# Kernel optimization log

Hardware: AMD Instinct MI355X
Metric: run time of the kernel (lower is better)

Reference implementation:

```python
import jax, jax.numpy as jnp
import numpy as np

B, S, D = 1, 2048, 6144
H, KV, HD = 48, 8, 128  # query heads, kv heads, head dim
THETA = 10000.0


def _rope_tables(seq_len, head_dim, theta):
    pos = jnp.arange(seq_len, dtype=jnp.float32)
    inv_freq = 1.0 / (theta ** (jnp.arange(0, head_dim, 2, dtype=jnp.float32) / head_dim))
    freqs = pos[:, None] * inv_freq[None, :]                 # [S, HD/2]
    emb = jnp.concatenate([freqs, freqs], axis=-1)           # [S, HD]
    return jnp.cos(emb), jnp.sin(emb)


def setup_inputs() -> dict:
    key = jax.random.key(0)
    k1, k2, k3 = jax.random.split(key, 3)
    hidden_states = jax.random.normal(k1, (B, S, D), dtype=jnp.float32) * 0.02
    w_qkv = jax.random.normal(k2, (D, (H + 2 * KV) * HD), dtype=jnp.float32) * 0.02
    w_out = jax.random.normal(k3, (H * HD, D), dtype=jnp.float32) * 0.02
    cos, sin = _rope_tables(S, HD, THETA)
    return {"hidden_states": hidden_states, "cos": cos, "sin": sin,
            "w_qkv": w_qkv, "w_out": w_out}


def _rotate_half(x):
    x1, x2 = jnp.split(x, 2, axis=-1)
    return jnp.concatenate([-x2, x1], axis=-1)


def reference(hidden_states, cos, sin, w_qkv, w_out):
    b, s, d = hidden_states.shape
    # fused QKV projection
    qkv = jnp.einsum('bsd,de->bse', hidden_states, w_qkv)
    q = qkv[..., : H * HD].reshape(b, s, H, HD)
    k = qkv[..., H * HD: (H + KV) * HD].reshape(b, s, KV, HD)
    v = qkv[..., (H + KV) * HD:].reshape(b, s, KV, HD)
    # rotary embedding (rotate-half form)
    c = cos[None, :, None, :]
    sn = sin[None, :, None, :]
    q = q * c + _rotate_half(q) * sn
    k = k * c + _rotate_half(k) * sn
    # GQA: expand kv heads to query heads
    rep = H // KV
    k = jnp.repeat(k, rep, axis=2)  # [b, s, H, HD]
    v = jnp.repeat(v, rep, axis=2)
    scale = 1.0 / jnp.sqrt(jnp.float32(HD))
    scores = jnp.einsum('bqhd,bkhd->bhqk', q, k) * scale     # [b,H,S,S]
    causal = jnp.tril(jnp.ones((s, s), dtype=bool))
    scores = jnp.where(causal[None, None], scores, jnp.float32(-1e30))
    attn = jax.nn.softmax(scores, axis=-1)
    out = jnp.einsum('bhqk,bkhd->bqhd', attn, v).reshape(b, s, H * HD)
    return jnp.einsum('bsd,de->bse', out, w_out)
```

## Files before the change

kernel.cpp:

```cpp
#include <hip/hip_runtime.h>


#define S_   2048
#define D_   6144
#define H_   48
#define KV_  8
#define HD_  128
#define NQK  8192
#define REP  6

typedef __attribute__((ext_vector_type(8)))  __bf16 bf16x8;
typedef __attribute__((ext_vector_type(4)))  __bf16 bf16x4;
typedef __attribute__((ext_vector_type(2)))  __bf16 bf16x2;
typedef __attribute__((ext_vector_type(4)))  float  f32x4;
typedef __attribute__((ext_vector_type(16))) float  f32x16;
typedef __attribute__((ext_vector_type(4)))  float  float4v;

__device__ __forceinline__ void gl_lds16(const void* g, void* l) {
  __builtin_amdgcn_global_load_lds(
      (const __attribute__((address_space(1))) void*)g,
      (__attribute__((address_space(3))) void*)l, 16, 0, 0);
}

__device__ __forceinline__ unsigned pack2(float a, float b) {
  union { bf16x2 v; unsigned u; } x;
  x.v[0] = (__bf16)a; x.v[1] = (__bf16)b;
  return x.u;
}

__global__ __launch_bounds__(256) void cvt_bf16(const float* __restrict__ in,
                                                __bf16* __restrict__ out, int n4) {
  int stride = gridDim.x * 256;
  for (int i = blockIdx.x * 256 + threadIdx.x; i < n4; i += stride) {
    float4v v = ((const float4v*)in)[i];
    bf16x4 o;
    o[0] = (__bf16)v[0]; o[1] = (__bf16)v[1];
    o[2] = (__bf16)v[2]; o[3] = (__bf16)v[3];
    ((bf16x4*)out)[i] = o;
  }
}

__global__ __launch_bounds__(256) void wtrans(const float* __restrict__ src,
                                              __bf16* __restrict__ dst,
                                              int K, int N) {
  __shared__ float t[64][37];
  const int n0 = blockIdx.x * 32, k0 = blockIdx.y * 64;
  const int tid = threadIdx.x;
  const int kr = tid >> 3, nc = (tid & 7) * 4;
#pragma unroll
  for (int i = 0; i < 2; ++i) {
    float4v v = *(const float4v*)(src + (size_t)(k0 + kr + i * 32) * N + n0 + nc);
    t[kr + i * 32][nc + 0] = v[0];
    t[kr + i * 32][nc + 1] = v[1];
    t[kr + i * 32][nc + 2] = v[2];
    t[kr + i * 32][nc + 3] = v[3];
  }
  __syncthreads();
  const int nr = tid >> 3, kc = (tid & 7) * 8;
  bf16x8 o;
#pragma unroll
  for (int j = 0; j < 8; ++j) o[j] = (__bf16)t[kc + j][nr];
  *(bf16x8*)(dst + (size_t)(n0 + nr) * K + k0 + kc) = o;
}

template <typename CT, int BN>
__global__ __launch_bounds__(512, 2) void gemm_bt(const __bf16* __restrict__ A,
                                                  const __bf16* __restrict__ BT,
                                                  CT* __restrict__ C,
                                                  int M, int N, int K) {
  constexpr int NB = BN / 64;
  constexpr int NF = BN / 64;
  __shared__ __align__(16) __bf16 As[2][256 * 64];
  __shared__ __align__(16) __bf16 Bs[2][BN * 64];
  const int tid = threadIdx.x;
  const int w = tid >> 6, l = tid & 63;
  const int lr = l & 15, lg = l >> 4;
  const int wm = w >> 2, wn = w & 3;
  const int nwg = gridDim.x * gridDim.y;
  int bid = blockIdx.y * gridDim.x + blockIdx.x;
  bid = (bid & 7) * (nwg >> 3) + (bid >> 3);
  const int m0 = (bid / gridDim.x) * 256, n0 = (bid % gridDim.x) * BN;
  const int nkt = K >> 6;

  auto stage_all = [&](int T) {
    const int buf = T & 1, k0 = T << 6;
#pragma unroll
    for (int j = 0; j < 4; ++j) {
      int idx = j * 512 + tid;
      int row = idx >> 3;
      int c = (idx & 7) ^ (row & 7);
      gl_lds16(A + (size_t)(m0 + row) * K + k0 + c * 8,
               As[buf] + (size_t)(j * 512 + w * 64) * 8);
    }
#pragma unroll
    for (int j = 0; j < NB; ++j) {
      int idx = j * 512 + tid;
      int row = idx >> 3;
      int c = (idx & 7) ^ (row & 7);
      gl_lds16(BT + (size_t)(n0 + row) * K + k0 + c * 8,
               Bs[buf] + (size_t)(j * 512 + w * 64) * 8);
    }
  };
  auto rdA = [&](const __bf16* Ab, int mh, int kk, bf16x8* afr) {
#pragma unroll
    for (int m = 0; m < 4; ++m) {
      int row = wm * 128 + (mh * 4 + m) * 16 + lr;
      afr[m] = *(const bf16x8*)(Ab + (size_t)row * 64
                                + (((kk * 4 + lg) ^ (lr & 7)) * 8));
    }
  };
  auto rdB = [&](const __bf16* Bb, int kk, bf16x8* bfr) {
#pragma unroll
    for (int n = 0; n < NF; ++n) {
      int row = wn * (BN / 4) + n * 16 + lr;
      bfr[n] = *(const bf16x8*)(Bb + (size_t)row * 64
                                + (((kk * 4 + lg) ^ (lr & 7)) * 8));
    }
  };
#define SBAR  __builtin_amdgcn_s_barrier()
#define MFMA_CLUSTER(ACC_OFF)                                                   \
  __builtin_amdgcn_s_setprio(1);                                               \
  _Pragma("unroll")                                                             \
  for (int m = 0; m < 4; ++m)                                                   \
    _Pragma("unroll")                                                           \
    for (int n = 0; n < NF; ++n)                                                \
      acc[(ACC_OFF) + m][n] = __builtin_amdgcn_mfma_f32_16x16x32_bf16(          \
          afr[m], bfr[n], acc[(ACC_OFF) + m][n], 0, 0, 0);                      \
  __builtin_amdgcn_s_setprio(0)

  f32x4 acc[8][NF] = {};
  stage_all(0);
  asm volatile("s_waitcnt vmcnt(0)" ::: "memory");
  SBAR;

  for (int T = 0; T < nkt; ++T) {
    const __bf16* Ab = As[T & 1];
    const __bf16* Bb = Bs[T & 1];
    bf16x8 afr[4], bfr[NF];
    rdA(Ab, 0, 0, afr);
    rdB(Bb, 0, bfr);
    if (T + 1 < nkt) stage_all(T + 1);
    MFMA_CLUSTER(0);
    SBAR;
    rdA(Ab, 1, 0, afr);
    MFMA_CLUSTER(4);
    SBAR;
    rdA(Ab, 0, 1, afr);
    rdB(Bb, 1, bfr);
    MFMA_CLUSTER(0);
    SBAR;
    rdA(Ab, 1, 1, afr);
    MFMA_CLUSTER(4);
    asm volatile("s_waitcnt lgkmcnt(0)" ::: "memory");
    if (T + 1 < nkt) asm volatile("s_waitcnt vmcnt(0)" ::: "memory");
    SBAR;
  }
#undef SBAR
#undef MFMA_CLUSTER
#pragma unroll
  for (int m = 0; m < 8; ++m)
#pragma unroll
    for (int n = 0; n < NF; ++n)
#pragma unroll
      for (int j = 0; j < 4; ++j) {
        int row = m0 + wm * 128 + m * 16 + lg * 4 + j;
        int col = n0 + wn * (BN / 4) + n * 16 + lr;
        C[(size_t)row * N + col] = (CT)acc[m][n][j];
      }
}

template <typename CT>
__global__ __launch_bounds__(512, 2) void gemm2_bt(const __bf16* __restrict__ A,
                                                   const __bf16* __restrict__ BT,
                                                   CT* __restrict__ C,
                                                   int M, int N, int K) {
  __shared__ __align__(16) __bf16 As[2][128 * 64];
  __shared__ __align__(16) __bf16 Bs[2][192 * 64];
  const int tid = threadIdx.x;
  const int w = tid >> 6, l = tid & 63;
  const int lr = l & 15, lg = l >> 4;
  const int wm = w >> 2, wn = w & 3;
  const int nwg = gridDim.x * gridDim.y;
  int bid = blockIdx.y * gridDim.x + blockIdx.x;
  bid = (bid & 7) * (nwg >> 3) + (bid >> 3);
  const int m0 = (bid / gridDim.x) * 128, n0 = (bid % gridDim.x) * 192;
  const int nkt = K >> 6;

  auto stage_all = [&](int T) {
    const int buf = T & 1, k0 = T << 6;
#pragma unroll
    for (int j = 0; j < 2; ++j) {
      int idx = j * 512 + tid;
      int row = idx >> 3;
      int c = (idx & 7) ^ (row & 7);
      gl_lds16(A + (size_t)(m0 + row) * K + k0 + c * 8,
               As[buf] + (size_t)(j * 512 + w * 64) * 8);
    }
#pragma unroll
    for (int j = 0; j < 3; ++j) {
      int idx = j * 512 + tid;
      int row = idx >> 3;
      int c = (idx & 7) ^ (row & 7);
      gl_lds16(BT + (size_t)(n0 + row) * K + k0 + c * 8,
               Bs[buf] + (size_t)(j * 512 + w * 64) * 8);
    }
  };
  auto rdA = [&](const __bf16* Ab, int kk, bf16x8* afr) {
#pragma unroll
    for (int m = 0; m < 4; ++m) {
      int row = wm * 64 + m * 16 + lr;
      afr[m] = *(const bf16x8*)(Ab + (size_t)row * 64
                                + (((kk * 4 + lg) ^ (lr & 7)) * 8));
    }
  };
  auto rdB = [&](const __bf16* Bb, int kk, bf16x8* bfr) {
#pragma unroll
    for (int n = 0; n < 3; ++n) {
      int row = wn * 48 + n * 16 + lr;
      bfr[n] = *(const bf16x8*)(Bb + (size_t)row * 64
                                + (((kk * 4 + lg) ^ (lr & 7)) * 8));
    }
  };

  f32x4 acc[4][3] = {};
  stage_all(0);
  asm volatile("s_waitcnt vmcnt(0)" ::: "memory");
  __builtin_amdgcn_s_barrier();

  for (int T = 0; T < nkt; ++T) {
    const __bf16* Ab = As[T & 1];
    const __bf16* Bb = Bs[T & 1];
    bf16x8 afr[4], bfr[3];
    rdA(Ab, 0, afr);
    rdB(Bb, 0, bfr);
    if (T + 1 < nkt) stage_all(T + 1);
    __builtin_amdgcn_s_setprio(1);
#pragma unroll
    for (int m = 0; m < 4; ++m)
#pragma unroll
      for (int n = 0; n < 3; ++n)
        acc[m][n] = __builtin_amdgcn_mfma_f32_16x16x32_bf16(afr[m], bfr[n], acc[m][n], 0, 0, 0);
    __builtin_amdgcn_s_setprio(0);
    __builtin_amdgcn_s_barrier();
    rdA(Ab, 1, afr);
    rdB(Bb, 1, bfr);
    __builtin_amdgcn_s_setprio(1);
#pragma unroll
    for (int m = 0; m < 4; ++m)
#pragma unroll
      for (int n = 0; n < 3; ++n)
        acc[m][n] = __builtin_amdgcn_mfma_f32_16x16x32_bf16(afr[m], bfr[n], acc[m][n], 0, 0, 0);
    __builtin_amdgcn_s_setprio(0);
    asm volatile("s_waitcnt lgkmcnt(0)" ::: "memory");
    if (T + 1 < nkt) asm volatile("s_waitcnt vmcnt(0)" ::: "memory");
    __builtin_amdgcn_s_barrier();
  }
#pragma unroll
  for (int m = 0; m < 4; ++m)
#pragma unroll
    for (int n = 0; n < 3; ++n)
#pragma unroll
      for (int j = 0; j < 4; ++j) {
        int row = m0 + wm * 64 + m * 16 + lg * 4 + j;
        int col = n0 + wn * 48 + n * 16 + lr;
        C[(size_t)row * N + col] = (CT)acc[m][n][j];
      }
}

__global__ __launch_bounds__(256) void rope_qk(const __bf16* __restrict__ qkv,
                                               const float* __restrict__ cosT,
                                               const float* __restrict__ sinT,
                                               __bf16* __restrict__ Qo,
                                               __bf16* __restrict__ Ko) {
  const int s = blockIdx.x;
  const __bf16* base = qkv + (size_t)s * NQK;
  const float* ct = cosT + s * HD_;
  const float* st = sinT + s * HD_;
  const float scale = 0.1275174313f;
  for (int q4 = threadIdx.x; q4 < H_ * HD_ / 4; q4 += 256) {
    int h = q4 >> 5, d = (q4 & 31) * 4;
    bf16x4 x  = *(const bf16x4*)(base + h * HD_ + d);
    bf16x4 xr = (d < 64) ? *(const bf16x4*)(base + h * HD_ + d + 64)
                         : *(const bf16x4*)(base + h * HD_ + d - 64);
    float4v c4 = *(const float4v*)(ct + d);
    float4v s4 = *(const float4v*)(st + d);
    bf16x4 o;
#pragma unroll
    for (int j = 0; j < 4; ++j) {
      float r = (d < 64) ? -(float)xr[j] : (float)xr[j];
      o[j] = (__bf16)(((float)x[j] * c4[j] + r * s4[j]) * scale);
    }
    *(bf16x4*)(Qo + ((size_t)s * H_ + h) * HD_ + d) = o;
  }
  for (int q4 = threadIdx.x; q4 < KV_ * HD_ / 4; q4 += 256) {
    int h = q4 >> 5, d = (q4 & 31) * 4;
    const __bf16* kb = base + H_ * HD_;
    bf16x4 x  = *(const bf16x4*)(kb + h * HD_ + d);
    bf16x4 xr = (d < 64) ? *(const bf16x4*)(kb + h * HD_ + d + 64)
                         : *(const bf16x4*)(kb + h * HD_ + d - 64);
    float4v c4 = *(const float4v*)(ct + d);
    float4v s4 = *(const float4v*)(st + d);
    bf16x4 o;
#pragma unroll
    for (int j = 0; j < 4; ++j) {
      float r = (d < 64) ? -(float)xr[j] : (float)xr[j];
      o[j] = (__bf16)((float)x[j] * c4[j] + r * s4[j]);
    }
    *(bf16x4*)(Ko + ((size_t)s * KV_ + h) * HD_ + d) = o;
  }
}

__global__ __launch_bounds__(256) void v_trans(const __bf16* __restrict__ qkv,
                                               __bf16* __restrict__ Vt) {
  __shared__ __bf16 t[32][36];
  const int s0 = blockIdx.x * 32, d0 = blockIdx.y * 32, h = blockIdx.z;
  const int tx = threadIdx.x, ty = threadIdx.y;
  *(bf16x4*)&t[ty][tx * 4] =
      *(const bf16x4*)(qkv + (size_t)(s0 + ty) * NQK + (H_ + KV_) * HD_ + h * HD_ + d0 + tx * 4);
  __syncthreads();
  bf16x4 o;
#pragma unroll
  for (int j = 0; j < 4; ++j) o[j] = t[tx * 4 + j][ty];
  *(bf16x4*)(Vt + ((size_t)h * HD_ + d0 + ty) * S_ + s0 + tx * 4) = o;
}

__global__ __launch_bounds__(256, 2) void attn(const __bf16* __restrict__ Q,
                                               const __bf16* __restrict__ Kb,
                                               const __bf16* __restrict__ Vt,
                                               __bf16* __restrict__ O) {
  __shared__ __align__(16) __bf16 Ks[2][64 * 128];
  __shared__ __align__(16) __bf16 Vs[2][128 * 64];
  const int bx = blockIdx.x, h = blockIdx.y, kvh = h / REP;
  const int tid = threadIdx.x, w = tid >> 6, l = tid & 63;
  const int c = l & 31, g = l >> 5;
  const int qb = bx * 128;
  const int qrow = qb + w * 32 + c;
  const int tmax_w = (qb + w * 32 + 31) >> 6;
  const int NT = (qb >> 6) + 2;

  auto stage = [&](int t) {
    const int buf = t & 1;
    const int kbase = t << 6;
#pragma unroll
    for (int j = 0; j < 4; ++j) {
      int idx = j * 256 + tid;
      int row = idx >> 4, cc = (idx & 15) ^ (row & 15);
      gl_lds16(Kb + ((size_t)(kbase + row) * KV_ + kvh) * HD_ + cc * 8,
               Ks[buf] + (size_t)(j * 256 + w * 64) * 8);
    }
#pragma unroll
    for (int j = 0; j < 4; ++j) {
      int idx = j * 256 + tid;
      int row = idx >> 3, cc = (idx & 7) ^ (row & 7);
      gl_lds16(Vt + (size_t)(kvh * HD_ + row) * S_ + kbase + cc * 8,
               Vs[buf] + (size_t)(j * 256 + w * 64) * 8);
    }
  };

  bf16x8 qf[8];
  const __bf16* qp = Q + ((size_t)qrow * H_ + h) * HD_ + g * 8;
#pragma unroll
  for (int st = 0; st < 8; ++st) qf[st] = *(const bf16x8*)(qp + st * 16);

  f32x16 o[4] = {};
  float m = -1e30f, lsum = 0.f;

  stage(0);
  __syncthreads();
  for (int t = 0; t < NT; ++t) {
    const int buf = t & 1;
    if (t + 1 < NT) stage(t + 1);
    if (t <= tmax_w) {
      const int kbase = t << 6;
      f32x16 s0 = {}, s1 = {};
      __builtin_amdgcn_s_setprio(1);
#pragma unroll
      for (int st = 0; st < 8; ++st) {
        int ch = ((st * 2 + g) ^ (c & 15)) * 8;
        bf16x8 k0 = *(const bf16x8*)(Ks[buf] + (size_t)c * 128 + ch);
        bf16x8 k1 = *(const bf16x8*)(Ks[buf] + (size_t)(32 + c) * 128 + ch);
        s0 = __builtin_amdgcn_mfma_f32_32x32x16_bf16(k0, qf[st], s0, 0, 0, 0);
        s1 = __builtin_amdgcn_mfma_f32_32x32x16_bf16(k1, qf[st], s1, 0, 0, 0);
      }
      __builtin_amdgcn_s_setprio(0);
      if (t == tmax_w) {
#pragma unroll
        for (int r = 0; r < 16; ++r) {
          int krow = (r & 3) + 8 * (r >> 2) + 4 * g;
          if (kbase + krow > qrow)      s0[r] = -1e30f;
          if (kbase + 32 + krow > qrow) s1[r] = -1e30f;
        }
      }
      float mj = s0[0];
#pragma unroll
      for (int r = 1; r < 16; ++r) mj = fmaxf(mj, s0[r]);
#pragma unroll
      for (int r = 0; r < 16; ++r) mj = fmaxf(mj, s1[r]);
      mj = fmaxf(mj, __shfl_xor(mj, 32));
      float mnew = fmaxf(m, mj);
      float sc = __builtin_amdgcn_exp2f(m - mnew);
      float rs = 0.f;
      float p0[16], p1[16];
#pragma unroll
      for (int r = 0; r < 16; ++r) { p0[r] = __builtin_amdgcn_exp2f(s0[r] - mnew); rs += p0[r]; }
#pragma unroll
      for (int r = 0; r < 16; ++r) { p1[r] = __builtin_amdgcn_exp2f(s1[r] - mnew); rs += p1[r]; }
      rs += __shfl_xor(rs, 32);
      lsum = lsum * sc + rs;
      m = mnew;
#pragma unroll
      for (int db = 0; db < 4; ++db)
#pragma unroll
        for (int r = 0; r < 16; ++r) o[db][r] *= sc;
      unsigned bq[4][4];
#pragma unroll
      for (int n = 0; n < 2; ++n)
#pragma unroll
        for (int tq = 0; tq < 2; ++tq) {
          const float* pp = n ? p1 : p0;
          unsigned q0 = pack2(pp[8 * tq + 0], pp[8 * tq + 1]);
          unsigned q1 = pack2(pp[8 * tq + 2], pp[8 * tq + 3]);
          unsigned q2 = pack2(pp[8 * tq + 4], pp[8 * tq + 5]);
          unsigned q3 = pack2(pp[8 * tq + 6], pp[8 * tq + 7]);
          unsigned v0 = g ? q0 : q2;
          unsigned v1 = g ? q1 : q3;
          unsigned sh0 = (unsigned)__shfl_xor((int)v0, 32);
          unsigned sh1 = (unsigned)__shfl_xor((int)v1, 32);
          int s = n * 2 + tq;
          bq[s][0] = g ? sh0 : q0;
          bq[s][1] = g ? sh1 : q1;
          bq[s][2] = g ? q2 : sh0;
          bq[s][3] = g ? q3 : sh1;
        }
      __builtin_amdgcn_s_setprio(1);
#pragma unroll
      for (int s = 0; s < 4; ++s) {
        union { unsigned u[4]; bf16x8 v; } bb;
        bb.u[0] = bq[s][0]; bb.u[1] = bq[s][1]; bb.u[2] = bq[s][2]; bb.u[3] = bq[s][3];
#pragma unroll
        for (int db = 0; db < 4; ++db) {
          int ch = ((s * 2 + g) ^ (c & 7)) * 8;
          bf16x8 vfr = *(const bf16x8*)(Vs[buf] + (size_t)(db * 32 + c) * 64 + ch);
          o[db] = __builtin_amdgcn_mfma_f32_32x32x16_bf16(vfr, bb.v, o[db], 0, 0, 0);
        }
      }
      __builtin_amdgcn_s_setprio(0);
    }
    if (t + 1 < NT) __syncthreads();
  }
  float inv = 1.f / lsum;
#pragma unroll
  for (int db = 0; db < 4; ++db)
#pragma unroll
    for (int rg = 0; rg < 4; ++rg) {
      bf16x4 ov;
#pragma unroll
      for (int j = 0; j < 4; ++j) ov[j] = (__bf16)(o[db][rg * 4 + j] * inv);
      *(bf16x4*)(O + (size_t)qrow * D_ + h * HD_ + db * 32 + rg * 8 + g * 4) = ov;
    }
}

extern "C" void kernel_launch(void* const* d_in, const int* in_sizes, int n_in,
                              void* d_out, int out_size, void* d_ws, size_t ws_size,
                              hipStream_t stream) {
  const float* hidden = (const float*)d_in[0];
  const float* cosT   = (const float*)d_in[1];
  const float* sinT   = (const float*)d_in[2];
  const float* w_qkv  = (const float*)d_in[3];
  const float* w_out  = (const float*)d_in[4];
  float* out = (float*)d_out;
  char* ws = (char*)d_ws;

  __bf16* wT   = (__bf16*)ws;
  __bf16* hb   = (__bf16*)(ws + 100663296);
  __bf16* qkvb = (__bf16*)(ws + 100663296 + 25165824);
  __bf16* q_b  = (__bf16*)(ws + 100663296 + 25165824 + 33554432);
  __bf16* k_b  = q_b + (size_t)S_ * H_ * HD_;
  __bf16* vt_b = k_b + (size_t)S_ * KV_ * HD_;

  cvt_bf16<<<dim3(2048), dim3(256), 0, stream>>>(hidden, hb, (int)((size_t)S_ * D_ / 4));
  wtrans<<<dim3(NQK / 32, D_ / 64), dim3(256), 0, stream>>>(w_qkv, wT, D_, NQK);
  gemm_bt<__bf16, 256><<<dim3(NQK / 256, S_ / 256), dim3(512), 0, stream>>>(hb, wT, qkvb, S_, NQK, D_);
  rope_qk<<<dim3(S_), dim3(256), 0, stream>>>(qkvb, cosT, sinT, q_b, k_b);
  v_trans<<<dim3(S_ / 32, HD_ / 32, KV_), dim3(8, 32), 0, stream>>>(qkvb, vt_b);
  wtrans<<<dim3(D_ / 32, D_ / 64), dim3(256), 0, stream>>>(w_out, wT, D_, D_);
  attn<<<dim3(S_ / 128, H_), dim3(256), 0, stream>>>(q_b, k_b, vt_b, hb);
  gemm2_bt<float><<<dim3(D_ / 192, S_ / 128), dim3(512), 0, stream>>>(hb, wT, out, S_, D_, D_);
}
```

Measured before the change: 628.4 us.

## Restructure QKV GEMM into 8-phase half-K staged pipeline

Replaces the QKV projection GEMM with a variant that splits each 64-wide K tile into two 32-wide halves, each in its own LDS buffer. Loads for later tiles are issued in finer-grained pieces across eight MFMA phases per two K tiles, waiting with vmcnt(4) instead of draining all loads. The LDS swizzle changes to fit 32-element rows. The goal is to keep more global loads in flight and overlap them better with MFMA work, at the cost of more barriers per iteration and more complex synchronisation.

```diff
diff --git a/kernel.cpp b/kernel.cpp
--- a/kernel.cpp
+++ b/kernel.cpp
@@ -63,15 +63,13 @@
   *(bf16x8*)(dst + (size_t)(n0 + nr) * K + k0 + kc) = o;
 }
 
-template <typename CT, int BN>
-__global__ __launch_bounds__(512, 2) void gemm_bt(const __bf16* __restrict__ A,
-                                                  const __bf16* __restrict__ BT,
-                                                  CT* __restrict__ C,
-                                                  int M, int N, int K) {
-  constexpr int NB = BN / 64;
-  constexpr int NF = BN / 64;
-  __shared__ __align__(16) __bf16 As[2][256 * 64];
-  __shared__ __align__(16) __bf16 Bs[2][BN * 64];
+template <typename CT>
+__global__ __launch_bounds__(512, 2) void gemm8p(const __bf16* __restrict__ A,
+                                                 const __bf16* __restrict__ BT,
+                                                 CT* __restrict__ C,
+                                                 int M, int N, int K) {
+  __shared__ __align__(16) __bf16 As[2][2][256 * 32];
+  __shared__ __align__(16) __bf16 Bs[2][2][256 * 32];
   const int tid = threadIdx.x;
   const int w = tid >> 6, l = tid & 63;
   const int lr = l & 15, lg = l >> 4;
@@ -79,92 +77,107 @@
   const int nwg = gridDim.x * gridDim.y;
   int bid = blockIdx.y * gridDim.x + blockIdx.x;
   bid = (bid & 7) * (nwg >> 3) + (bid >> 3);
-  const int m0 = (bid / gridDim.x) * 256, n0 = (bid % gridDim.x) * BN;
+  const int m0 = (bid / gridDim.x) * 256, n0 = (bid % gridDim.x) * 256;
   const int nkt = K >> 6;
 
-  auto stage_all = [&](int T) {
-    const int buf = T & 1, k0 = T << 6;
-#pragma unroll
-    for (int j = 0; j < 4; ++j) {
+  auto stageh = [&](int T, int mat, int kh) {
+    const __bf16* src = mat ? BT : A;
+    const int base0 = mat ? n0 : m0;
+    __bf16* dst = mat ? Bs[T & 1][kh] : As[T & 1][kh];
+    const int k0 = (T << 6) + (kh << 5);
+#pragma unroll
+    for (int j = 0; j < 2; ++j) {
       int idx = j * 512 + tid;
-      int row = idx >> 3;
-      int c = (idx & 7) ^ (row & 7);
-      gl_lds16(A + (size_t)(m0 + row) * K + k0 + c * 8,
-               As[buf] + (size_t)(j * 512 + w * 64) * 8);
-    }
-#pragma unroll
-    for (int j = 0; j < NB; ++j) {
-      int idx = j * 512 + tid;
-      int row = idx >> 3;
-      int c = (idx & 7) ^ (row & 7);
-      gl_lds16(BT + (size_t)(n0 + row) * K + k0 + c * 8,
-               Bs[buf] + (size_t)(j * 512 + w * 64) * 8);
-    }
-  };
-  auto rdA = [&](const __bf16* Ab, int mh, int kk, bf16x8* afr) {
+      int row = idx >> 2;
+      int sc = (idx & 3) ^ ((row >> 1) & 3);
+      gl_lds16(src + (size_t)(base0 + row) * K + k0 + sc * 8,
+               dst + (size_t)(j * 512 + w * 64) * 8);
+    }
+  };
+  auto rdA4 = [&](int buf, int ks, int mh, bf16x8* afr) {
 #pragma unroll
     for (int m = 0; m < 4; ++m) {
-      int row = wm * 128 + (mh * 4 + m) * 16 + lr;
-      afr[m] = *(const bf16x8*)(Ab + (size_t)row * 64
-                                + (((kk * 4 + lg) ^ (lr & 7)) * 8));
-    }
-  };
-  auto rdB = [&](const __bf16* Bb, int kk, bf16x8* bfr) {
-#pragma unroll
-    for (int n = 0; n < NF; ++n) {
-      int row = wn * (BN / 4) + n * 16 + lr;
-      bfr[n] = *(const bf16x8*)(Bb + (size_t)row * 64
-                                + (((kk * 4 + lg) ^ (lr & 7)) * 8));
+      int row = wm * 128 + mh * 64 + m * 16 + lr;
+      afr[m] = *(const bf16x8*)(&As[buf][ks][(size_t)row * 32
+                                + ((lg ^ ((row >> 1) & 3)) * 8)]);
+    }
+  };
+  auto rdB4 = [&](int buf, int ks, bf16x8* bfr) {
+#pragma unroll
+    for (int n = 0; n < 4; ++n) {
+      int row = wn * 64 + n * 16 + lr;
+      bfr[n] = *(const bf16x8*)(&Bs[buf][ks][(size_t)row * 32
+                                + ((lg ^ ((row >> 1) & 3)) * 8)]);
     }
   };
 #define SBAR  __builtin_amdgcn_s_barrier()
-#define MFMA_CLUSTER(ACC_OFF)                                                   \
+#define LGKM0 asm volatile("s_waitcnt lgkmcnt(0)" ::: "memory")
+#define MFMA16(MH)                                                              \
   __builtin_amdgcn_s_setprio(1);                                               \
   _Pragma("unroll")                                                             \
   for (int m = 0; m < 4; ++m)                                                   \
     _Pragma("unroll")                                                           \
-    for (int n = 0; n < NF; ++n)                                                \
-      acc[(ACC_OFF) + m][n] = __builtin_amdgcn_mfma_f32_16x16x32_bf16(          \
-          afr[m], bfr[n], acc[(ACC_OFF) + m][n], 0, 0, 0);                      \
+    for (int n = 0; n < 4; ++n)                                                 \
+      acc[(MH) * 4 + m][n] = __builtin_amdgcn_mfma_f32_16x16x32_bf16(           \
+          afr[m], bfr[n], acc[(MH) * 4 + m][n], 0, 0, 0);                       \
   __builtin_amdgcn_s_setprio(0)
 
-  f32x4 acc[8][NF] = {};
-  stage_all(0);
-  asm volatile("s_waitcnt vmcnt(0)" ::: "memory");
+  f32x4 acc[8][4] = {};
+  stageh(0, 0, 0); stageh(0, 1, 0); stageh(0, 0, 1); stageh(0, 1, 1);
+  stageh(1, 0, 0); stageh(1, 1, 0);
+  asm volatile("s_waitcnt vmcnt(4)" ::: "memory");
   SBAR;
 
-  for (int T = 0; T < nkt; ++T) {
-    const __bf16* Ab = As[T & 1];
-    const __bf16* Bb = Bs[T & 1];
-    bf16x8 afr[4], bfr[NF];
-    rdA(Ab, 0, 0, afr);
-    rdB(Bb, 0, bfr);
-    if (T + 1 < nkt) stage_all(T + 1);
-    MFMA_CLUSTER(0);
-    SBAR;
-    rdA(Ab, 1, 0, afr);
-    MFMA_CLUSTER(4);
-    SBAR;
-    rdA(Ab, 0, 1, afr);
-    rdB(Bb, 1, bfr);
-    MFMA_CLUSTER(0);
-    SBAR;
-    rdA(Ab, 1, 1, afr);
-    MFMA_CLUSTER(4);
-    asm volatile("s_waitcnt lgkmcnt(0)" ::: "memory");
-    if (T + 1 < nkt) asm volatile("s_waitcnt vmcnt(0)" ::: "memory");
-    SBAR;
+  for (int t = 0; t < nkt; t += 2) {
+    const int u = t + 1, v = t + 2, x = t + 3;
+    const int bt = t & 1, bu = u & 1;
+    bf16x8 afr[4], bfr[4];
+    rdA4(bt, 0, 0, afr); rdB4(bt, 0, bfr);
+    stageh(u, 0, 1);
+    SBAR; LGKM0; MFMA16(0); SBAR;
+    rdA4(bt, 0, 1, afr);
+    stageh(u, 1, 1);
+    SBAR; LGKM0; MFMA16(1); SBAR;
+    rdA4(bt, 1, 0, afr); rdB4(bt, 1, bfr);
+    if (v < nkt) stageh(v, 0, 0);
+    SBAR; LGKM0; MFMA16(0); SBAR;
+    rdA4(bt, 1, 1, afr);
+    if (v < nkt) {
+      stageh(v, 1, 0);
+      asm volatile("s_waitcnt vmcnt(4)" ::: "memory");
+    } else {
+      asm volatile("s_waitcnt vmcnt(0)" ::: "memory");
+    }
+    SBAR; LGKM0; MFMA16(1); SBAR;
+    rdA4(bu, 0, 0, afr); rdB4(bu, 0, bfr);
+    if (v < nkt) stageh(v, 0, 1);
+    SBAR; LGKM0; MFMA16(0); SBAR;
+    rdA4(bu, 0, 1, afr);
+    if (v < nkt) stageh(v, 1, 1);
+    SBAR; LGKM0; MFMA16(1); SBAR;
+    rdA4(bu, 1, 0, afr); rdB4(bu, 1, bfr);
+    if (x < nkt) stageh(x, 0, 0);
+    SBAR; LGKM0; MFMA16(0); SBAR;
+    rdA4(bu, 1, 1, afr);
+    if (x < nkt) {
+      stageh(x, 1, 0);
+      asm volatile("s_waitcnt vmcnt(4)" ::: "memory");
+    } else {
+      asm volatile("s_waitcnt vmcnt(0)" ::: "memory");
+    }
+    SBAR; LGKM0; MFMA16(1); SBAR;
   }
 #undef SBAR
-#undef MFMA_CLUSTER
+#undef LGKM0
+#undef MFMA16
 #pragma unroll
   for (int m = 0; m < 8; ++m)
 #pragma unroll
-    for (int n = 0; n < NF; ++n)
+    for (int n = 0; n < 4; ++n)
 #pragma unroll
       for (int j = 0; j < 4; ++j) {
         int row = m0 + wm * 128 + m * 16 + lg * 4 + j;
-        int col = n0 + wn * (BN / 4) + n * 16 + lr;
+        int col = n0 + wn * 64 + n * 16 + lr;
         C[(size_t)row * N + col] = (CT)acc[m][n][j];
       }
 }
@@ -480,7 +493,7 @@
 
   cvt_bf16<<<dim3(2048), dim3(256), 0, stream>>>(hidden, hb, (int)((size_t)S_ * D_ / 4));
   wtrans<<<dim3(NQK / 32, D_ / 64), dim3(256), 0, stream>>>(w_qkv, wT, D_, NQK);
-  gemm_bt<__bf16, 256><<<dim3(NQK / 256, S_ / 256), dim3(512), 0, stream>>>(hb, wT, qkvb, S_, NQK, D_);
+  gemm8p<__bf16><<<dim3(NQK / 256, S_ / 256), dim3(512), 0, stream>>>(hb, wT, qkvb, S_, NQK, D_);
   rope_qk<<<dim3(S_), dim3(256), 0, stream>>>(qkvb, cosT, sinT, q_b, k_b);
   v_trans<<<dim3(S_ / 32, HD_ / 32, KV_), dim3(8, 32), 0, stream>>>(qkvb, vt_b);
   wtrans<<<dim3(D_ / 32, D_ / 64), dim3(256), 0, stream>>>(w_out, wT, D_, D_);
```

New measurement: 639.0 us. Within noise of the previous version (+1.7%).
